# Optimization experiments

Measured on AMD Instinct MI355X. Metric: run time of the kernel, lower is better.

The kernel has to match this reference:

```python
import jax, jax.numpy as jnp
import numpy as np

B, N, FD, H = 8, 256, 1024, 256
RATIO, TEMP = 0.6, 0.5


def setup_inputs() -> dict:
    key = jax.random.key(0)
    ks = jax.random.split(key, 5)
    x = jax.random.normal(ks[0], (B, N, FD), dtype=jnp.float32)
    s1 = 1.0 / np.sqrt(2 * FD)
    W1 = jax.random.uniform(ks[1], (H, 2 * FD), minval=-s1, maxval=s1, dtype=jnp.float32)
    b1 = jax.random.uniform(ks[2], (H,), minval=-s1, maxval=s1, dtype=jnp.float32)
    s2 = 1.0 / np.sqrt(H)
    W2 = jax.random.uniform(ks[3], (1, H), minval=-s2, maxval=s2, dtype=jnp.float32)
    b2 = jax.random.uniform(ks[4], (1,), minval=-s2, maxval=s2, dtype=jnp.float32)
    return {"x": x, "W1": W1, "b1": b1, "W2": W2, "b2": b2}


def reference(x, W1, b1, W2, b2):
    Bb, Nn, Fd = x.shape
    # Linear on cat([row, col]) == row @ W1[:, :F].T + col @ W1[:, F:].T + b1,
    # so project nodes once and broadcast-add instead of materializing [N,N,2F].
    pr = jnp.einsum('bnf,hf->bnh', x, W1[:, :Fd])  # row projections
    pc = jnp.einsum('bnf,hf->bnh', x, W1[:, Fd:])  # col projections
    h = jax.nn.relu(pr[:, :, None, :] + pc[:, None, :, :] + b1)  # [B,N,N,H]
    edge_scores = jnp.einsum('bijh,h->bij', h, W2[0]) + b2[0]    # [B,N,N]
    flat = edge_scores.reshape(Bb, Nn * Nn)
    soft_mask = jax.nn.softmax(flat / TEMP, axis=1)
    k = int(RATIO * Nn * Nn)
    topk_vals, _ = jax.lax.top_k(soft_mask, k)
    threshold = topk_vals[:, -1:]
    causal_mask = jnp.where(soft_mask >= threshold, soft_mask, jnp.zeros_like(soft_mask))
    causal_mask = causal_mask / (causal_mask.sum(axis=1, keepdims=True) + 1e-12)
    conf_mask = 1.0 - causal_mask
    causal_adj = causal_mask.reshape(Bb, Nn, Nn)
    conf_adj = conf_mask.reshape(Bb, Nn, Nn)
    return (causal_adj, conf_adj, edge_scores, soft_mask)
```

## Files before the change

kernel.cpp:

```cpp
#include <hip/hip_runtime.h>

#define BB 8
#define NN 256
#define FDIM 1024
#define HDIM 256
#define NSQ 65536
#define ROWS 2048
#define KSEL 39321
#define NBIN 8192
#define LDSW 72

typedef short s16x8 __attribute__((ext_vector_type(8)));
typedef float f32x4 __attribute__((ext_vector_type(4)));
typedef float f32x2 __attribute__((ext_vector_type(2)));

__device__ __forceinline__ unsigned fkey(float f) {
  unsigned u = __float_as_uint(f);
  return (u & 0x80000000u) ? ~u : (u | 0x80000000u);
}
__device__ __forceinline__ float finv(unsigned k) {
  unsigned u = (k & 0x80000000u) ? (k & 0x7fffffffu) : ~k;
  return __uint_as_float(u);
}
__device__ __forceinline__ unsigned short f2bf(float f) {
  unsigned u = __float_as_uint(f);
  unsigned r = (u + 0x7fffu + ((u >> 16) & 1u)) >> 16;
  return (unsigned short)r;
}

__global__ __launch_bounds__(256) void k_prep(const float* __restrict__ X,
                                              const float* __restrict__ W1,
                                              unsigned short* __restrict__ XB,
                                              unsigned short* __restrict__ W1B,
                                              unsigned* __restrict__ zero) {
  const int bx = blockIdx.x, t = threadIdx.x;
  if (bx < 1280) {
    const float* src = (bx < 1024) ? X : W1;
    unsigned short* dst = (bx < 1024) ? XB : W1B;
    const int idx = ((bx < 1024 ? bx : bx - 1024) * 256 + t) * 8;
    float4 v0 = *(const float4*)&src[idx];
    float4 v1 = *(const float4*)&src[idx + 4];
    s16x8 o;
    o[0] = (short)f2bf(v0.x); o[1] = (short)f2bf(v0.y); o[2] = (short)f2bf(v0.z); o[3] = (short)f2bf(v0.w);
    o[4] = (short)f2bf(v1.x); o[5] = (short)f2bf(v1.y); o[6] = (short)f2bf(v1.z); o[7] = (short)f2bf(v1.w);
    *(s16x8*)&dst[idx] = o;
  } else {
    const int idx = ((bx - 1280) * 256 + t) * 4;
    *(uint4*)&zero[idx] = make_uint4(0u, 0u, 0u, 0u);
  }
}

__global__ __launch_bounds__(256) void k_gemm(const unsigned short* __restrict__ XB,
                                              const unsigned short* __restrict__ W1B,
                                              const float* __restrict__ b1,
                                              float* __restrict__ PRBT,
                                              float* __restrict__ PCT) {
  const int bm = blockIdx.x * 64;
  const int bn = blockIdx.y * 32;
  const int t = threadIdx.x;
  __shared__ short As[64 * LDSW];
  __shared__ short Bs[32 * LDSW];
  const int sr = t >> 2, cg = t & 3;
  const unsigned short* pa = XB + (bm + sr) * FDIM + cg * 16;
  const int srb = t >> 3, cgb = t & 7;
  const unsigned short* pb = (bn < 256)
      ? (W1B + (bn + srb) * (2 * FDIM) + cgb * 8)
      : (W1B + (bn - 256 + srb) * (2 * FDIM) + FDIM + cgb * 8);
  const int w = t >> 6, lane = t & 63;
  const int wm = (w & 1) * 32, wn = (w >> 1) * 16;
  const int q = lane >> 4, m16 = lane & 15;
  f32x4 acc[2] = {};
  s16x8 ra0 = *(const s16x8*)(pa);
  s16x8 ra1 = *(const s16x8*)(pa + 8);
  s16x8 rb = *(const s16x8*)(pb);
  for (int k0 = 0; k0 < FDIM; k0 += 64) {
    __syncthreads();
    *(s16x8*)&As[sr * LDSW + cg * 16]     = ra0;
    *(s16x8*)&As[sr * LDSW + cg * 16 + 8] = ra1;
    *(s16x8*)&Bs[srb * LDSW + cgb * 8]    = rb;
    if (k0 + 64 < FDIM) {
      ra0 = *(const s16x8*)(pa + k0 + 64);
      ra1 = *(const s16x8*)(pa + k0 + 72);
      rb  = *(const s16x8*)(pb + k0 + 64);
    }
    __syncthreads();
#pragma unroll
    for (int koff = 0; koff < 64; koff += 32) {
      s16x8 af0 = *(s16x8*)&As[(wm + m16) * LDSW + koff + q * 8];
      s16x8 af1 = *(s16x8*)&As[(wm + 16 + m16) * LDSW + koff + q * 8];
      s16x8 bf0 = *(s16x8*)&Bs[(wn + m16) * LDSW + koff + q * 8];
      acc[0] = __builtin_amdgcn_mfma_f32_16x16x32_bf16(af0, bf0, acc[0], 0, 0, 0);
      acc[1] = __builtin_amdgcn_mfma_f32_16x16x32_bf16(af1, bf0, acc[1], 0, 0, 0);
    }
  }
#pragma unroll
  for (int rt = 0; rt < 2; ++rt) {
    const int hn = bn + wn + m16;
    const int row0 = bm + wm + rt * 16 + q * 4;
    if (hn < 256) {
      const float bias = b1[hn];
      float4 v = make_float4(acc[rt][0] + bias, acc[rt][1] + bias,
                             acc[rt][2] + bias, acc[rt][3] + bias);
      *(float4*)&PRBT[hn * ROWS + row0] = v;
    } else {
      float4 v = make_float4(acc[rt][0], acc[rt][1], acc[rt][2], acc[rt][3]);
      *(float4*)&PCT[(hn - 256) * ROWS + row0] = v;
    }
  }
}

__global__ __launch_bounds__(512) void k_edge(const float* __restrict__ PRBT,
                                              const float* __restrict__ PCT,
                                              const float* __restrict__ W2,
                                              const float* __restrict__ b2,
                                              float* __restrict__ edge,
                                              unsigned* __restrict__ gcount,
                                              float* __restrict__ gvsum) {
  const int b = blockIdx.z;
  const int i0 = blockIdx.y * 64, j0 = blockIdx.x * 32;
  const int t = threadIdx.x;
  __shared__ float prs[64][68];
  __shared__ float pcs[64][36];
  __shared__ float w2s[HDIM];
  __shared__ unsigned lhc[NBIN / 2];
  __shared__ float lhv[NBIN];
  if (t < HDIM) w2s[t] = W2[t];
#pragma unroll
  for (int i = 0; i < 2; ++i) ((uint4*)lhc)[t + i * 512] = make_uint4(0u, 0u, 0u, 0u);
#pragma unroll
  for (int i = 0; i < 4; ++i) ((float4*)lhv)[t + i * 512] = make_float4(0.f, 0.f, 0.f, 0.f);
  const float bias = b2[0];
  const int tmi = t >> 4, tnj = t & 15;
  f32x2 acc0 = {0.f, 0.f};
  f32x2 acc1 = {0.f, 0.f};
  for (int h0 = 0; h0 < HDIM; h0 += 64) {
    __syncthreads();
#pragma unroll
    for (int s = 0; s < 2; ++s) {
      int idx = t + s * 512;
      int hh = idx >> 4, ig = idx & 15;
      *(float4*)&prs[hh][ig * 4] =
          *(const float4*)&PRBT[(h0 + hh) * ROWS + b * NN + i0 + ig * 4];
    }
    {
      int hh = t >> 3, jg = t & 7;
      *(float4*)&pcs[hh][jg * 4] =
          *(const float4*)&PCT[(h0 + hh) * ROWS + b * NN + j0 + jg * 4];
    }
    __syncthreads();
#pragma unroll 8
    for (int h = 0; h < 64; ++h) {
      const float w = w2s[h0 + h];
      const f32x2 a = *(const f32x2*)&prs[h][tmi * 2];
      const f32x2 c = *(const f32x2*)&pcs[h][tnj * 2];
      f32x2 x0 = c + a.x;
      f32x2 x1 = c + a.y;
      x0.x = fmaxf(x0.x, 0.f); x0.y = fmaxf(x0.y, 0.f);
      x1.x = fmaxf(x1.x, 0.f); x1.y = fmaxf(x1.y, 0.f);
      acc0 += x0 * w;
      acc1 += x1 * w;
    }
  }
  const int ibase = i0 + tmi * 2, jbase = j0 + tnj * 2;
  float av[2][2] = {{acc0.x, acc0.y}, {acc1.x, acc1.y}};
#pragma unroll
  for (int i = 0; i < 2; ++i) {
    float2 v = make_float2(av[i][0] + bias, av[i][1] + bias);
    *(float2*)&edge[b * NSQ + (ibase + i) * NN + jbase] = v;
    float ex = __expf(v.x * 2.f), ey = __expf(v.y * 2.f);
    unsigned bx = fkey(v.x) >> 19, by = fkey(v.y) >> 19;
    atomicAdd(&lhc[bx >> 1], 1u << ((bx & 1) * 16));
    atomicAdd(&lhv[bx], ex);
    atomicAdd(&lhc[by >> 1], 1u << ((by & 1) * 16));
    atomicAdd(&lhv[by], ey);
  }
  __syncthreads();
  unsigned* gc = gcount + b * NBIN;
  float* gv = gvsum + b * NBIN;
#pragma unroll
  for (int i = 0; i < 8; ++i) {
    const int idx = t + i * 512;
    unsigned wv = lhc[idx];
    if (wv) {
      unsigned lo = wv & 0xFFFFu, hi = wv >> 16;
      if (lo) atomicAdd(&gc[2 * idx], lo);
      if (hi) atomicAdd(&gc[2 * idx + 1], hi);
    }
  }
#pragma unroll
  for (int i = 0; i < 16; ++i) {
    const int idx = t + i * 512;
    float vv = lhv[idx];
    if (vv != 0.f) atomicAdd(&gv[idx], vv);
  }
}

__global__ __launch_bounds__(256) void k_out(const float* __restrict__ edge,
                                             const unsigned* __restrict__ gcount,
                                             const float* __restrict__ gvsum,
                                             float* __restrict__ soft,
                                             float* __restrict__ causal,
                                             float* __restrict__ conf) {
  const int b = blockIdx.y;
  const int t = threadIdx.x;
  __shared__ unsigned S[256];
  __shared__ float V[256];
  __shared__ unsigned ou[1];
  __shared__ float of[3];
  const unsigned* hc = gcount + b * NBIN;
  const float* hv = gvsum + b * NBIN;
  unsigned cs = 0; float vs = 0.f;
  {
    const uint4* hc4 = (const uint4*)(hc + t * 32);
    const float4* hv4 = (const float4*)(hv + t * 32);
#pragma unroll
    for (int i = 0; i < 8; ++i) {
      uint4 c = hc4[i];
      float4 v = hv4[i];
      cs += c.x + c.y + c.z + c.w;
      vs += v.x + v.y + v.z + v.w;
    }
  }
  S[t] = cs; V[t] = vs;
  __syncthreads();
  for (int off = 1; off < 256; off <<= 1) {
    unsigned su = (t + off < 256) ? S[t + off] : 0u;
    float vu = (t + off < 256) ? V[t + off] : 0.f;
    __syncthreads();
    S[t] += su; V[t] += vu;
    __syncthreads();
  }
  if (t == 0) of[2] = V[0];
  const int above = (int)(S[t] - cs);
  if (above < KSEL && (int)S[t] >= KSEL) {
    int cum = above;
    float vcum = V[t] - vs;
    for (int i = 31; i >= 0; --i) {
      unsigned c = hc[t * 32 + i];
      float v = hv[t * 32 + i];
      cum += (int)c;
      if (cum >= KSEL) { ou[0] = (unsigned)(t * 32 + i); of[0] = vcum; of[1] = v; break; }
      vcum += v;
    }
  }
  __syncthreads();
  const float th = finv(ou[0] << 19);
  const float Z = of[2];
  const float invZ = 1.f / Z;
  const float msum = (of[0] + of[1]) * invZ;
  const float invD = 1.f / (msum + 1e-12f);
  const int off = b * NSQ + blockIdx.x * 2048 + t * 8;
#pragma unroll
  for (int i = 0; i < 8; i += 4) {
    float4 v = *(const float4*)&edge[off + i];
    float4 o = make_float4(__expf(v.x * 2.f) * invZ, __expf(v.y * 2.f) * invZ,
                           __expf(v.z * 2.f) * invZ, __expf(v.w * 2.f) * invZ);
    *(float4*)&soft[off + i] = o;
    float cx = v.x >= th ? o.x * invD : 0.f;
    float cy = v.y >= th ? o.y * invD : 0.f;
    float cz = v.z >= th ? o.z * invD : 0.f;
    float cw = v.w >= th ? o.w * invD : 0.f;
    *(float4*)&causal[off + i] = make_float4(cx, cy, cz, cw);
    *(float4*)&conf[off + i]   = make_float4(1.f - cx, 1.f - cy, 1.f - cz, 1.f - cw);
  }
}

extern "C" void kernel_launch(void* const* d_in, const int* in_sizes, int n_in,
                              void* d_out, int out_size, void* d_ws, size_t ws_size,
                              hipStream_t stream) {
  const float* x  = (const float*)d_in[0];
  const float* W1 = (const float*)d_in[1];
  const float* b1 = (const float*)d_in[2];
  const float* W2 = (const float*)d_in[3];
  const float* b2 = (const float*)d_in[4];

  float* out = (float*)d_out;
  float* causal = out;
  float* conf   = out + 1 * 524288;
  float* edge   = out + 2 * 524288;
  float* soft   = out + 3 * 524288;

  float* ws = (float*)d_ws;
  float*          PRBT   = ws;
  float*          PCT    = ws + 524288;
  unsigned short* XB     = (unsigned short*)(ws + 1048576);
  unsigned short* W1B    = (unsigned short*)(ws + 2097152);
  unsigned*       gcount = (unsigned*)(ws + 2359296);
  float*          gvsum  = (float*)(ws + 2424832);

  k_prep<<<1408, 256, 0, stream>>>(x, W1, XB, W1B, gcount);
  k_gemm<<<dim3(32, 16), 256, 0, stream>>>(XB, W1B, b1, PRBT, PCT);
  k_edge<<<dim3(8, 4, 8), 512, 0, stream>>>(PRBT, PCT, W2, b2, edge, gcount, gvsum);
  k_out<<<dim3(32, 8), 256, 0, stream>>>(edge, gcount, gvsum, soft, causal, conf);
}
```

Measured before the change: 105.7 us.

## Use direct global-to-LDS loads with double buffering and XOR swizzle in GEMM

The projection GEMM now loads tiles straight from global memory into LDS with global_load_lds, double-buffered so the next K-slice is fetched while MFMAs run on the current one. The padded LDS layout is replaced by an XOR-swizzled 64-wide layout to avoid bank conflicts, and one barrier per iteration is removed. LDS use doubles, and correctness depends on the async LDS writes being complete at the single barrier.

```diff
diff --git a/kernel.cpp b/kernel.cpp
--- a/kernel.cpp
+++ b/kernel.cpp
@@ -8,7 +8,6 @@
 #define ROWS 2048
 #define KSEL 39321
 #define NBIN 8192
-#define LDSW 72
 
 typedef short s16x8 __attribute__((ext_vector_type(8)));
 typedef float f32x4 __attribute__((ext_vector_type(4)));
@@ -26,6 +25,11 @@
   unsigned u = __float_as_uint(f);
   unsigned r = (u + 0x7fffu + ((u >> 16) & 1u)) >> 16;
   return (unsigned short)r;
+}
+__device__ __forceinline__ void gl_lds16(const unsigned short* g, unsigned short* l) {
+  __builtin_amdgcn_global_load_lds(
+      (const __attribute__((address_space(1))) unsigned int*)(g),
+      (__attribute__((address_space(3))) unsigned int*)(l), 16, 0, 0);
 }
 
 __global__ __launch_bounds__(256) void k_prep(const float* __restrict__ X,
@@ -58,40 +62,44 @@
   const int bm = blockIdx.x * 64;
   const int bn = blockIdx.y * 32;
   const int t = threadIdx.x;
-  __shared__ short As[64 * LDSW];
-  __shared__ short Bs[32 * LDSW];
-  const int sr = t >> 2, cg = t & 3;
-  const unsigned short* pa = XB + (bm + sr) * FDIM + cg * 16;
-  const int srb = t >> 3, cgb = t & 7;
-  const unsigned short* pb = (bn < 256)
-      ? (W1B + (bn + srb) * (2 * FDIM) + cgb * 8)
-      : (W1B + (bn - 256 + srb) * (2 * FDIM) + FDIM + cgb * 8);
+  __shared__ unsigned short As[2][4096];
+  __shared__ unsigned short Bs[2][2048];
   const int w = t >> 6, lane = t & 63;
+  const int l3 = lane >> 3, l7 = lane & 7;
+  const int csw = (l7 ^ l3) * 8;
+  const unsigned short* srcA0 = XB + (bm + w * 8 + l3) * FDIM + csw;
+  const unsigned short* srcA1 = XB + (bm + 32 + w * 8 + l3) * FDIM + csw;
+  const int rowB = w * 8 + l3;
+  const unsigned short* srcB = (bn < 256)
+      ? (W1B + (bn + rowB) * (2 * FDIM) + csw)
+      : (W1B + (bn - 256 + rowB) * (2 * FDIM) + FDIM + csw);
+  const int dst = w * 512 + lane * 8;
   const int wm = (w & 1) * 32, wn = (w >> 1) * 16;
   const int q = lane >> 4, m16 = lane & 15;
+  const int x7 = m16 & 7;
   f32x4 acc[2] = {};
-  s16x8 ra0 = *(const s16x8*)(pa);
-  s16x8 ra1 = *(const s16x8*)(pa + 8);
-  s16x8 rb = *(const s16x8*)(pb);
+  gl_lds16(srcA0, &As[0][dst]);
+  gl_lds16(srcA1, &As[0][2048 + dst]);
+  gl_lds16(srcB,  &Bs[0][dst]);
+  __syncthreads();
+  int cur = 0;
   for (int k0 = 0; k0 < FDIM; k0 += 64) {
-    __syncthreads();
-    *(s16x8*)&As[sr * LDSW + cg * 16]     = ra0;
-    *(s16x8*)&As[sr * LDSW + cg * 16 + 8] = ra1;
-    *(s16x8*)&Bs[srb * LDSW + cgb * 8]    = rb;
     if (k0 + 64 < FDIM) {
-      ra0 = *(const s16x8*)(pa + k0 + 64);
-      ra1 = *(const s16x8*)(pa + k0 + 72);
-      rb  = *(const s16x8*)(pb + k0 + 64);
-    }
-    __syncthreads();
+      gl_lds16(srcA0 + k0 + 64, &As[cur ^ 1][dst]);
+      gl_lds16(srcA1 + k0 + 64, &As[cur ^ 1][2048 + dst]);
+      gl_lds16(srcB  + k0 + 64, &Bs[cur ^ 1][dst]);
+    }
 #pragma unroll
     for (int koff = 0; koff < 64; koff += 32) {
-      s16x8 af0 = *(s16x8*)&As[(wm + m16) * LDSW + koff + q * 8];
-      s16x8 af1 = *(s16x8*)&As[(wm + 16 + m16) * LDSW + koff + q * 8];
-      s16x8 bf0 = *(s16x8*)&Bs[(wn + m16) * LDSW + koff + q * 8];
+      const int soff = ((((koff >> 5) * 4 + q) ^ x7)) * 8;
+      s16x8 af0 = *(s16x8*)&As[cur][(wm + m16) * 64 + soff];
+      s16x8 af1 = *(s16x8*)&As[cur][(wm + 16 + m16) * 64 + soff];
+      s16x8 bf0 = *(s16x8*)&Bs[cur][(wn + m16) * 64 + soff];
       acc[0] = __builtin_amdgcn_mfma_f32_16x16x32_bf16(af0, bf0, acc[0], 0, 0, 0);
       acc[1] = __builtin_amdgcn_mfma_f32_16x16x32_bf16(af1, bf0, acc[1], 0, 0, 0);
     }
+    __syncthreads();
+    cur ^= 1;
   }
 #pragma unroll
   for (int rt = 0; rt < 2; ++rt) {
```

Result: slower. 111.5 us (+5.5%).
